# Kernel tuning notes

Hardware: AMD Instinct MI355X
Metric: run time of the kernel (lower is better)

The kernel has to match this reference:

```python
import jax, jax.numpy as jnp
import numpy as np


def setup_inputs() -> dict:
    key = jax.random.key(0)
    k1, k2, k3 = jax.random.split(key, 3)
    bs, seqlen, hidden = 2, 2048, 1024
    s, h = 4, 256  # sqrt_n_heads, head_size
    std = 0.02
    num_layers = 12
    hidden_states = jax.random.normal(k1, (bs, seqlen, hidden), dtype=jnp.float32)
    q_scale = 1.0 / np.sqrt(2.0 * num_layers * h)
    queries = jax.random.normal(k2, (s, h, h * s), dtype=jnp.float32) * std * q_scale
    combiners = jax.random.normal(k3, (s, h * s, h), dtype=jnp.float32) * (std * q_scale)
    return {"hidden_states": hidden_states, "queries": queries, "combiners": combiners}


def reference(hidden_states, queries, combiners):
    # queries: [s1, h, s*h], combiners: [s1, s*h, h]
    s, h, _ = queries.shape
    bs, S, E = hidden_states.shape
    x = hidden_states.reshape(bs, S, s, h)            # [b, t, s, h]
    qw = queries.reshape(s, h, s, h)                  # [s1, h_in, s2, h_out]
    # projected queries, already permuted to [s2, b, t, s1, f]
    Q = jnp.einsum('btae,aeqf->qbtaf', x, qw)
    # pre-attention scores: [s2, b, t, s1, u] (u = key position)  ~O(S^2)
    pre = jnp.einsum('qbtaf,buqf->qbtau', Q, x)
    # attention output, permuted to [s1, b, t, s2, g]
    attn = jnp.einsum('qbtau,buqg->abtqg', pre, x)
    attn = attn.reshape(s, bs, S, s * h)              # [s1, b, t, s2*h]
    out = jnp.einsum('abtk,akg->btag', attn, combiners)
    return out.reshape(bs, S, s * h)
```

## Files before the change

### kernel.cpp

```cpp
#include <hip/hip_runtime.h>
#include <hip/hip_bf16.h>


typedef unsigned short u16;
using short8  = __attribute__((ext_vector_type(8))) short;
using floatx4 = __attribute__((ext_vector_type(4))) float;

__device__ inline u16 f2bf(float f) {
    unsigned u = __float_as_uint(f);
    unsigned r = u + 0x7fffu + ((u >> 16) & 1u);
    return (u16)(r >> 16);
}

template <typename T>
__device__ inline void stage64(const T* __restrict__ src, long ld,
                               u16* __restrict__ dst, int tid) {
#pragma unroll
    for (int it = 0; it < 4; ++it) {
        const int flat = (it * 256 + tid) * 4;
        const int kl = flat & 63, rl = flat >> 6;
        ushort4 v;
        if (sizeof(T) == 4) {
            const float4 f = *(const float4*)&((const float*)src)[(long)rl * ld + kl];
            v.x = f2bf(f.x); v.y = f2bf(f.y); v.z = f2bf(f.z); v.w = f2bf(f.w);
        } else {
            v = *(const ushort4*)&((const u16*)src)[(long)rl * ld + kl];
        }
        const int chunk = ((kl >> 5) * 4 + (rl >> 4)) * 64 + ((kl >> 3) & 3) * 16 + (rl & 15);
        *(ushort4*)&dst[chunk * 8 + (kl & 7)] = v;
    }
}

template <typename TA, typename TB, bool ATOMIC>
__device__ inline void gemm_tile(const TA* __restrict__ A, long lda,
                                 const TB* __restrict__ B, long ldb,
                                 float* __restrict__ C, long ldc,
                                 int K, int m0, int n0) {
    __shared__ u16 As[4096];
    __shared__ u16 Bs[4096];
    const int tid = threadIdx.x, lane = tid & 63, w = tid >> 6;
    const int IA = (w & 1) * 2, JB = (w >> 1) * 2;
    floatx4 acc[2][2] = {};

    for (int k0 = 0; k0 < K; k0 += 64) {
        stage64(A + k0, lda, As, tid);
        stage64(B + k0, ldb, Bs, tid);
        __syncthreads();
#pragma unroll
        for (int s = 0; s < 2; ++s) {
            short8 af[2], bfr[2];
#pragma unroll
            for (int i = 0; i < 2; ++i)
                af[i] = *(const short8*)&As[((s * 4 + IA + i) * 64 + lane) * 8];
#pragma unroll
            for (int j = 0; j < 2; ++j)
                bfr[j] = *(const short8*)&Bs[((s * 4 + JB + j) * 64 + lane) * 8];
#pragma unroll
            for (int i = 0; i < 2; ++i)
#pragma unroll
                for (int j = 0; j < 2; ++j)
                    acc[i][j] = __builtin_amdgcn_mfma_f32_16x16x32_bf16(af[i], bfr[j], acc[i][j], 0, 0, 0);
        }
        __syncthreads();
    }
    const int rb = (lane >> 4) * 4, col = lane & 15;
#pragma unroll
    for (int i = 0; i < 2; ++i)
#pragma unroll
        for (int j = 0; j < 2; ++j)
#pragma unroll
            for (int r = 0; r < 4; ++r) {
                const int gm = m0 + (IA + i) * 16 + rb + r;
                const int gn = n0 + (JB + j) * 16 + col;
                float* p = &C[(long)gm * ldc + gn];
                if (ATOMIC) atomicAdd(p, acc[i][j][r]); else *p = acc[i][j][r];
            }
}

__device__ inline void transpose64(const float* __restrict__ src, long lds_,
                                   int r0, int c0,
                                   u16* __restrict__ dst, long ldd,
                                   float (*tile)[65], int t) {
#pragma unroll
    for (int it = 0; it < 4; ++it) {
        const int row = (t >> 4) + it * 16, cq = (t & 15) * 4;
        *(float4*)&tile[row][cq] = *(const float4*)&src[(long)(r0 + row) * lds_ + c0 + cq];
    }
    __syncthreads();
#pragma unroll
    for (int it = 0; it < 4; ++it) {
        const int cl = (t >> 4) + it * 16, rq = (t & 15) * 4;
        ushort4 v;
        v.x = f2bf(tile[rq + 0][cl]); v.y = f2bf(tile[rq + 1][cl]);
        v.z = f2bf(tile[rq + 2][cl]); v.w = f2bf(tile[rq + 3][cl]);
        *(ushort4*)&dst[(long)(c0 + cl) * ldd + r0 + rq] = v;
    }
}

__global__ __launch_bounds__(256) void k_prep(const float* __restrict__ x,
                                              const float* __restrict__ comb,
                                              u16* __restrict__ xt,
                                              u16* __restrict__ cb,
                                              float* __restrict__ GZ) {
    __shared__ float tile[64][65];
    const int j = blockIdx.x, t = threadIdx.x;
    if (j < 1024) {
        const int b = j >> 9, local = j & 511;
        const int u0 = (local & 31) * 64, f0 = (local >> 5) * 64;
        transpose64(x + (long)b * 2097152, 1024, u0, f0,
                    xt + (long)b * 2097152, 2048, tile, t);
    } else if (j < 1280) {
        const int idx = j - 1024, a = idx >> 6, local = idx & 63;
        const int k0 = (local & 15) * 64, g0 = (local >> 4) * 64;
        transpose64(comb + (long)a * 262144, 256, k0, g0,
                    cb + (long)a * 262144, 1024, tile, t);
    } else {
        const int idx = j - 1280;
        float4 zero = {0.f, 0.f, 0.f, 0.f};
        float4* z = (float4*)GZ;
#pragma unroll
        for (int it = 0; it < 4; ++it)
            z[(long)idx * 1024 + it * 256 + t] = zero;
    }
}

__global__ __launch_bounds__(256) void k_gram(const u16* __restrict__ xt,
                                              float* __restrict__ G) {
    const int tile = blockIdx.x, bq = blockIdx.y, split = blockIdx.z;
    const int tm = tile >> 2, tn = tile & 3;
    const int b = bq >> 2, q = bq & 3;
    const u16* base = xt + (long)b * 2097152 + (long)q * 256 * 2048 + split * 256;
    gemm_tile<u16, u16, true>(base + (long)tm * 64 * 2048, 2048,
                              base + (long)tn * 64 * 2048, 2048,
                              G + (long)bq * 65536, 256,
                              256, tm * 64, tn * 64);
}

__global__ __launch_bounds__(256) void k_2a(const u16* __restrict__ cb,
                                            const float* __restrict__ G,
                                            float* __restrict__ Tt) {
    const int tile = blockIdx.x, i = blockIdx.y;
    const int tm = tile >> 2, tn = tile & 3;
    const int q = i & 3, ba = i >> 2, b = ba >> 2, a = ba & 3;
    gemm_tile<u16, float, false>(
        cb + (long)a * 262144 + (long)tm * 64 * 1024 + q * 256, 1024,
        G + (long)(b * 4 + q) * 65536 + (long)tn * 64 * 256, 256,
        Tt + (long)ba * 262144, 1024,
        256, tm * 64, q * 256 + tn * 64);
}

__global__ __launch_bounds__(256) void k_2b(const float* __restrict__ Tt,
                                            const float* __restrict__ qw,
                                            float* __restrict__ Wt) {
    const int tile = blockIdx.x, ba = blockIdx.y, split = blockIdx.z;
    const int tm = tile >> 2, tn = tile & 3;
    const int a = ba & 3;
    gemm_tile<float, float, true>(
        Tt + (long)ba * 262144 + (long)tm * 64 * 1024 + split * 256, 1024,
        qw + (long)a * 262144 + (long)tn * 64 * 1024 + split * 256, 1024,
        Wt + (long)ba * 65536, 256,
        256, tm * 64, tn * 64);
}

__global__ __launch_bounds__(256) void k_3(const float* __restrict__ x,
                                           const float* __restrict__ Wt,
                                           float* __restrict__ out) {
    const int tl = blockIdx.x, ba = blockIdx.y;
    const int tm = tl >> 2, tn = tl & 3;
    const int b = ba >> 2, a = ba & 3;
    gemm_tile<float, float, false>(
        x + (long)b * 2097152 + (long)tm * 64 * 1024 + a * 256, 1024,
        Wt + (long)ba * 65536 + (long)tn * 64 * 256, 256,
        out + (long)b * 2097152 + a * 256, 1024,
        256, tm * 64, tn * 64);
}

extern "C" void kernel_launch(void* const* d_in, const int* in_sizes, int n_in,
                              void* d_out, int out_size, void* d_ws, size_t ws_size,
                              hipStream_t stream) {
    const float* x    = (const float*)d_in[0];
    const float* qw   = (const float*)d_in[1];
    const float* comb = (const float*)d_in[2];
    float* out = (float*)d_out;

    char* ws = (char*)d_ws;
    float* G  = (float*)(ws);
    float* Wt = (float*)(ws + (2u << 20));
    float* Tt = (float*)(ws + (4u << 20));
    u16* xt   = (u16*)  (ws + (12u << 20));
    u16* cb   = (u16*)  (ws + (20u << 20));

    k_prep<<<1536, 256, 0, stream>>>(x, comb, xt, cb, G);
    k_gram<<<dim3(16, 8, 8), 256, 0, stream>>>(xt, G);
    k_2a  <<<dim3(16, 32),   256, 0, stream>>>(cb, G, Tt);
    k_2b  <<<dim3(16, 8, 4), 256, 0, stream>>>(Tt, qw, Wt);
    k_3   <<<dim3(128, 8),   256, 0, stream>>>(x, Wt, out);
}
```

Baseline: 143.9 us.

## Drop transpose prep kernel by staging K-major fp32 operands directly in GEMM

Removes the separate prep kernel that transposed x and combiners into bf16 scratch buffers. The Gram and T GEMMs now read the original fp32 tensors in K-major order and convert and scatter them into the MFMA shared-memory layout while staging. Zeroing of the accumulation buffers moves to hipMemsetAsync, which also clears Wt. This saves a kernel launch and a full extra read/write pass over x, but the new staging does 2-byte scalar LDS stores with likely bank conflicts and reads fp32 instead of bf16 in the Gram GEMM.

```diff
diff --git a/kernel.cpp b/kernel.cpp
--- a/kernel.cpp
+++ b/kernel.cpp
@@ -31,7 +31,23 @@
     }
 }
 
-template <typename TA, typename TB, bool ATOMIC>
+__device__ inline void stage_km64(const float* __restrict__ src, long ld,
+                                  u16* __restrict__ dst, int tid) {
+#pragma unroll
+    for (int it = 0; it < 4; ++it) {
+        const int flat = (it * 256 + tid) * 4;
+        const int m = flat & 63, k = flat >> 6;
+        const float4 f = *(const float4*)&src[(long)k * ld + m];
+        const int cb_ = ((k >> 5) * 4 + (m >> 4)) * 64 + ((k & 31) >> 3) * 16 + (m & 15);
+        const int j = k & 7;
+        dst[(cb_ + 0) * 8 + j] = f2bf(f.x);
+        dst[(cb_ + 1) * 8 + j] = f2bf(f.y);
+        dst[(cb_ + 2) * 8 + j] = f2bf(f.z);
+        dst[(cb_ + 3) * 8 + j] = f2bf(f.w);
+    }
+}
+
+template <typename TA, typename TB, bool AKM, bool BKM, bool ATOMIC>
 __device__ inline void gemm_tile(const TA* __restrict__ A, long lda,
                                  const TB* __restrict__ B, long ldb,
                                  float* __restrict__ C, long ldc,
@@ -43,8 +59,10 @@
     floatx4 acc[2][2] = {};
 
     for (int k0 = 0; k0 < K; k0 += 64) {
-        stage64(A + k0, lda, As, tid);
-        stage64(B + k0, ldb, Bs, tid);
+        if (AKM) stage_km64((const float*)A + (long)k0 * lda, lda, As, tid);
+        else     stage64(A + k0, lda, As, tid);
+        if (BKM) stage_km64((const float*)B + (long)k0 * ldb, ldb, Bs, tid);
+        else     stage64(B + k0, ldb, Bs, tid);
         __syncthreads();
 #pragma unroll
         for (int s = 0; s < 2; ++s) {
@@ -77,73 +95,27 @@
             }
 }
 
-__device__ inline void transpose64(const float* __restrict__ src, long lds_,
-                                   int r0, int c0,
-                                   u16* __restrict__ dst, long ldd,
-                                   float (*tile)[65], int t) {
-#pragma unroll
-    for (int it = 0; it < 4; ++it) {
-        const int row = (t >> 4) + it * 16, cq = (t & 15) * 4;
-        *(float4*)&tile[row][cq] = *(const float4*)&src[(long)(r0 + row) * lds_ + c0 + cq];
-    }
-    __syncthreads();
-#pragma unroll
-    for (int it = 0; it < 4; ++it) {
-        const int cl = (t >> 4) + it * 16, rq = (t & 15) * 4;
-        ushort4 v;
-        v.x = f2bf(tile[rq + 0][cl]); v.y = f2bf(tile[rq + 1][cl]);
-        v.z = f2bf(tile[rq + 2][cl]); v.w = f2bf(tile[rq + 3][cl]);
-        *(ushort4*)&dst[(long)(c0 + cl) * ldd + r0 + rq] = v;
-    }
-}
-
-__global__ __launch_bounds__(256) void k_prep(const float* __restrict__ x,
-                                              const float* __restrict__ comb,
-                                              u16* __restrict__ xt,
-                                              u16* __restrict__ cb,
-                                              float* __restrict__ GZ) {
-    __shared__ float tile[64][65];
-    const int j = blockIdx.x, t = threadIdx.x;
-    if (j < 1024) {
-        const int b = j >> 9, local = j & 511;
-        const int u0 = (local & 31) * 64, f0 = (local >> 5) * 64;
-        transpose64(x + (long)b * 2097152, 1024, u0, f0,
-                    xt + (long)b * 2097152, 2048, tile, t);
-    } else if (j < 1280) {
-        const int idx = j - 1024, a = idx >> 6, local = idx & 63;
-        const int k0 = (local & 15) * 64, g0 = (local >> 4) * 64;
-        transpose64(comb + (long)a * 262144, 256, k0, g0,
-                    cb + (long)a * 262144, 1024, tile, t);
-    } else {
-        const int idx = j - 1280;
-        float4 zero = {0.f, 0.f, 0.f, 0.f};
-        float4* z = (float4*)GZ;
-#pragma unroll
-        for (int it = 0; it < 4; ++it)
-            z[(long)idx * 1024 + it * 256 + t] = zero;
-    }
-}
-
-__global__ __launch_bounds__(256) void k_gram(const u16* __restrict__ xt,
+__global__ __launch_bounds__(256) void k_gram(const float* __restrict__ x,
                                               float* __restrict__ G) {
     const int tile = blockIdx.x, bq = blockIdx.y, split = blockIdx.z;
     const int tm = tile >> 2, tn = tile & 3;
     const int b = bq >> 2, q = bq & 3;
-    const u16* base = xt + (long)b * 2097152 + (long)q * 256 * 2048 + split * 256;
-    gemm_tile<u16, u16, true>(base + (long)tm * 64 * 2048, 2048,
-                              base + (long)tn * 64 * 2048, 2048,
-                              G + (long)bq * 65536, 256,
-                              256, tm * 64, tn * 64);
+    const float* base = x + (long)b * 2097152 + (long)split * 256 * 1024 + q * 256;
+    gemm_tile<float, float, true, true, true>(
+        base + tm * 64, 1024,
+        base + tn * 64, 1024,
+        G + (long)bq * 65536, 256,
+        256, tm * 64, tn * 64);
 }
 
-__global__ __launch_bounds__(256) void k_2a(const u16* __restrict__ cb,
+__global__ __launch_bounds__(256) void k_2a(const float* __restrict__ comb,
                                             const float* __restrict__ G,
                                             float* __restrict__ Tt) {
     const int tile = blockIdx.x, i = blockIdx.y;
     const int tm = tile >> 2, tn = tile & 3;
     const int q = i & 3, ba = i >> 2, b = ba >> 2, a = ba & 3;
-    gemm_tile<u16, float, false>(
-        cb + (long)a * 262144 + (long)tm * 64 * 1024 + q * 256, 1024,
+    gemm_tile<float, float, true, false, false>(
+        comb + (long)a * 262144 + (long)q * 256 * 256 + tm * 64, 256,
         G + (long)(b * 4 + q) * 65536 + (long)tn * 64 * 256, 256,
         Tt + (long)ba * 262144, 1024,
         256, tm * 64, q * 256 + tn * 64);
@@ -155,7 +127,7 @@
     const int tile = blockIdx.x, ba = blockIdx.y, split = blockIdx.z;
     const int tm = tile >> 2, tn = tile & 3;
     const int a = ba & 3;
-    gemm_tile<float, float, true>(
+    gemm_tile<float, float, false, false, true>(
         Tt + (long)ba * 262144 + (long)tm * 64 * 1024 + split * 256, 1024,
         qw + (long)a * 262144 + (long)tn * 64 * 1024 + split * 256, 1024,
         Wt + (long)ba * 65536, 256,
@@ -168,7 +140,7 @@
     const int tl = blockIdx.x, ba = blockIdx.y;
     const int tm = tl >> 2, tn = tl & 3;
     const int b = ba >> 2, a = ba & 3;
-    gemm_tile<float, float, false>(
+    gemm_tile<float, float, false, false, false>(
         x + (long)b * 2097152 + (long)tm * 64 * 1024 + a * 256, 1024,
         Wt + (long)ba * 65536 + (long)tn * 64 * 256, 256,
         out + (long)b * 2097152 + a * 256, 1024,
@@ -187,12 +159,10 @@
     float* G  = (float*)(ws);
     float* Wt = (float*)(ws + (2u << 20));
     float* Tt = (float*)(ws + (4u << 20));
-    u16* xt   = (u16*)  (ws + (12u << 20));
-    u16* cb   = (u16*)  (ws + (20u << 20));
 
-    k_prep<<<1536, 256, 0, stream>>>(x, comb, xt, cb, G);
-    k_gram<<<dim3(16, 8, 8), 256, 0, stream>>>(xt, G);
-    k_2a  <<<dim3(16, 32),   256, 0, stream>>>(cb, G, Tt);
+    hipMemsetAsync(d_ws, 0, 4u << 20, stream);
+    k_gram<<<dim3(16, 8, 8), 256, 0, stream>>>(x, G);
+    k_2a  <<<dim3(16, 32),   256, 0, stream>>>(comb, G, Tt);
     k_2b  <<<dim3(16, 8, 4), 256, 0, stream>>>(Tt, qw, Wt);
     k_3   <<<dim3(128, 8),   256, 0, stream>>>(x, Wt, out);
 }
```

Result: slower. 147.7 us (+2.7%).
